# Performance work log

Hardware: AMD Instinct MI355X
Metric: run time of the kernel (lower is better)

The kernel has to match this reference:

```python
import jax, jax.numpy as jnp
import numpy as np

MAX_ITER = 3  # matches init kwarg max_iter


def setup_inputs() -> dict:
    key = jax.random.key(0)
    k1, k2, k3, k4 = jax.random.split(key, 4)
    B, S = 4, 160
    return {
        "s_edge": jax.random.normal(k1, (B, S, S), dtype=jnp.float32),
        "s_sib": jax.random.normal(k2, (B, S, S, S), dtype=jnp.float32),
        "s_cop": jax.random.normal(k3, (B, S, S, S), dtype=jnp.float32),
        "s_grd": jax.random.normal(k4, (B, S, S, S), dtype=jnp.float32),
        "mask": jnp.ones((B, S, S), dtype=bool),
    }


def reference(s_edge, s_sib, s_cop, s_grd, mask):
    B, S, _ = mask.shape
    idx = jnp.arange(S)
    # Permute to the [head, mod, (sib), batch] layout used by the torch code.
    mask_p = jnp.transpose(mask, (2, 1, 0))              # [h, m, B]
    # 2nd-order mask: both (h,m) and (h,t) arcs valid, and t != h, t != m
    pair_ok = mask_p[:, None, :, :] & mask_p[:, :, None, :]   # [h, m, t, B]
    t_ok = (idx[:, None, None] != idx[None, None, :]) & (
        idx[None, :, None] != idx[None, None, :])             # [h, m, t]
    mask2o = (pair_ok & t_ok[..., None]).astype(s_edge.dtype)  # [h, m, t, B]

    se = jnp.transpose(s_edge, (2, 1, 0))                 # [h, m, B]
    ss = jnp.transpose(s_sib, (2, 1, 3, 0)) * mask2o      # [h, m, t, B]
    sc = jnp.transpose(s_cop, (2, 1, 3, 0)) * mask2o
    sg = jnp.transpose(s_grd, (2, 1, 3, 0)) * mask2o

    q = jnp.zeros((2, S, S, B), dtype=se.dtype)
    for _ in range(MAX_ITER):
        q1 = jax.nn.softmax(q, axis=0)[1]                 # [h, m, B]
        # f[h,m,b] = sum_t q1[h,t,b]*ss + q1[t,m,b]*sc + q1[m,t,b]*sg
        f = (jnp.einsum('htb,hmtb->hmb', q1, ss)
             + jnp.einsum('tmb,hmtb->hmb', q1, sc)
             + jnp.einsum('mtb,hmtb->hmb', q1, sg))
        q = jnp.stack([jnp.zeros_like(f), se + f])        # [2, h, m, B]

    logQ = jax.nn.log_softmax(jnp.transpose(q, (3, 2, 1, 0)), axis=-1)  # [B, m, h... -> B,S,S,2]
    return jnp.exp(logQ)
```

## Files before the change

kernel.cpp:

```cpp
#include <hip/hip_runtime.h>
#include <cmath>

constexpr int S = 160;
constexpr int BATCH = 4;
constexpr int ZSPLIT = 2;
constexpr int ROWS = S / ZSPLIT;
constexpr int KC = S / 4;
constexpr int CHUNKS = ROWS * KC;
constexpr int TPB = 256;
constexpr int FULL_STEPS = CHUNKS / TPB;
constexpr int TAIL = CHUNKS - FULL_STEPS * TPB;

__device__ __forceinline__ float sigmoidf_(float x) {
  return 1.0f / (1.0f + expf(-x));
}

__global__ void prep_wf(const int* __restrict__ mask, unsigned char* __restrict__ wf) {
  int i = blockIdx.x * blockDim.x + threadIdx.x;
  if (i >= BATCH * S * S) return;
  int t = i % S;
  int bh = i / S;
  int h = bh % S;
  int b = bh / S;
  wf[i] = (mask[(b * S + t) * S + h] != 0 && t != h) ? 1 : 0;
}

template <bool FIRST, bool LAST>
__global__ __launch_bounds__(TPB, 5) void mfvi_iter(
    const float* __restrict__ s_edge,
    const float* __restrict__ s_sib,
    const float* __restrict__ s_cop,
    const float* __restrict__ s_grd,
    const int* __restrict__ mask,
    const unsigned char* __restrict__ wf,
    const float* __restrict__ q1_in,
    float* __restrict__ q1_out,
    float* __restrict__ outp) {
  const int m = blockIdx.x;
  const int b = blockIdx.y;
  const int z = blockIdx.z;
  const int tid = threadIdx.x;

  __shared__ __align__(16) float part[CHUNKS];
  __shared__ __align__(16) float colm[S];
  __shared__ __align__(16) float rowm[S];
  __shared__ float sef[ROWS];
  __shared__ float pmf[ROWS];

  const float* G = q1_in + (size_t)b * S * S;
  const size_t bm = (size_t)b * S + m;
  const int h0 = z * ROWS;

  if (tid < S) {
    if (!FIRST) {
      colm[tid] = G[tid * S + m];
      rowm[tid] = G[m * S + tid];
    }
    if (tid < ROWS) {
      sef[tid] = s_edge[bm * S + h0 + tid];
      pmf[tid] = (mask[bm * S + h0 + tid] != 0) ? 1.0f : 0.0f;
    }
  }
  __syncthreads();

  const size_t blk = (bm * S + h0) * (size_t)S;
  const float4* SS = (const float4*)(s_sib + blk);
  const float4* CC = (const float4*)(s_cop + blk);
  const float4* GG = (const float4*)(s_grd + blk);
  const float4* QQ = (const float4*)(G + h0 * S);
  const unsigned* WF = (const unsigned*)(wf + ((size_t)b * S + h0) * S);
  const int msel = m >> 2;
  const unsigned mclr = ~(255u << ((m & 3) * 8));

  auto body = [&](int c) {
    unsigned wu = WF[c];
    float4 s = SS[c];
    float4 cv = CC[c];
    float4 g = GG[c];
    int k = c % KC;
    if (k == msel) wu &= mclr;
    float w0 = (float)(wu & 255u);
    float w1 = (float)((wu >> 8) & 255u);
    float w2 = (float)((wu >> 16) & 255u);
    float w3 = (float)(wu >> 24);
    float p;
    if (FIRST) {
      float t0 = s.x + cv.x + g.x;
      float t1 = s.y + cv.y + g.y;
      float t2 = s.z + cv.z + g.z;
      float t3 = s.w + cv.w + g.w;
      p = fmaf(w0, t0, fmaf(w1, t1, fmaf(w2, t2, w3 * t3)));
    } else {
      float4 q = QQ[c];
      float4 cm = ((const float4*)colm)[k];
      float4 rm = ((const float4*)rowm)[k];
      float t0 = fmaf(q.x, s.x, fmaf(cm.x, cv.x, rm.x * g.x));
      float t1 = fmaf(q.y, s.y, fmaf(cm.y, cv.y, rm.y * g.y));
      float t2 = fmaf(q.z, s.z, fmaf(cm.z, cv.z, rm.z * g.z));
      float t3 = fmaf(q.w, s.w, fmaf(cm.w, cv.w, rm.w * g.w));
      p = fmaf(w0, t0, fmaf(w1, t1, fmaf(w2, t2, w3 * t3)));
    }
    part[c] = p;
  };

  for (int step = 0; step < FULL_STEPS; ++step) body(step * TPB + tid);
  if (tid < TAIL) body(FULL_STEPS * TPB + tid);
  __syncthreads();

  if (tid < ROWS) {
    const float4* pr = (const float4*)part + tid * (KC / 4);
    float4 a = pr[0];
#pragma unroll
    for (int i = 1; i < KC / 4; ++i) {
      float4 v = pr[i];
      a.x += v.x; a.y += v.y; a.z += v.z; a.w += v.w;
    }
    float acc = (a.x + a.y) + (a.z + a.w);
    const int h = h0 + tid;
    const float qv = fmaf(pmf[tid], FIRST ? 0.5f * acc : acc, sef[tid]);
    if (!LAST) {
      q1_out[((size_t)b * S + h) * S + m] = sigmoidf_(qv);
    } else {
      float2 o;
      o.x = sigmoidf_(-qv);
      o.y = sigmoidf_(qv);
      ((float2*)outp)[bm * S + h] = o;
    }
  }
}

extern "C" void kernel_launch(void* const* d_in, const int* in_sizes, int n_in,
                              void* d_out, int out_size, void* d_ws, size_t ws_size,
                              hipStream_t stream) {
  const float* s_edge = (const float*)d_in[0];
  const float* s_sib = (const float*)d_in[1];
  const float* s_cop = (const float*)d_in[2];
  const float* s_grd = (const float*)d_in[3];
  const int* mask = (const int*)d_in[4];
  float* outp = (float*)d_out;

  const int qn = BATCH * S * S;
  float* q1A = (float*)d_ws;
  float* q1B = q1A + qn;
  unsigned char* wf = (unsigned char*)(q1B + qn);

  prep_wf<<<(qn + 255) / 256, 256, 0, stream>>>(mask, wf);

  dim3 grid(S, BATCH, ZSPLIT);
  mfvi_iter<true, false><<<grid, TPB, 0, stream>>>(
      s_edge, s_sib, s_cop, s_grd, mask, wf, q1A, q1B, nullptr);
  mfvi_iter<false, false><<<grid, TPB, 0, stream>>>(
      s_edge, s_sib, s_cop, s_grd, mask, wf, q1B, q1A, nullptr);
  mfvi_iter<false, true><<<grid, TPB, 0, stream>>>(
      s_edge, s_sib, s_cop, s_grd, mask, wf, q1A, nullptr, outp);
}
```

Measured before the change: 261.2 us.

## Split rows four ways, pad reduction buffer, and batch paired streaming loads

Doubles the row split per (m, batch) so each block handles 40 rows, doubling the grid to 2560 blocks, and raises the launch-bounds occupancy hint from 5 to 8 blocks. Pads each row of the partial-sum shared buffer so the per-row float4 reduction reads hit fewer LDS bank conflicts. Unrolls the streaming loop so two chunks' loads are issued before either is computed, raising memory-level parallelism. In exchange, register pressure rises under the tighter occupancy bound, each block does less work, and the colm/rowm setup is repeated by twice as many blocks.

```diff
diff --git a/kernel.cpp b/kernel.cpp
--- a/kernel.cpp
+++ b/kernel.cpp
@@ -3,9 +3,10 @@
 
 constexpr int S = 160;
 constexpr int BATCH = 4;
-constexpr int ZSPLIT = 2;
+constexpr int ZSPLIT = 4;
 constexpr int ROWS = S / ZSPLIT;
 constexpr int KC = S / 4;
+constexpr int PSTR = KC + 4;
 constexpr int CHUNKS = ROWS * KC;
 constexpr int TPB = 256;
 constexpr int FULL_STEPS = CHUNKS / TPB;
@@ -26,7 +27,7 @@
 }
 
 template <bool FIRST, bool LAST>
-__global__ __launch_bounds__(TPB, 5) void mfvi_iter(
+__global__ __launch_bounds__(TPB, 8) void mfvi_iter(
     const float* __restrict__ s_edge,
     const float* __restrict__ s_sib,
     const float* __restrict__ s_cop,
@@ -41,7 +42,7 @@
   const int z = blockIdx.z;
   const int tid = threadIdx.x;
 
-  __shared__ __align__(16) float part[CHUNKS];
+  __shared__ __align__(16) float part[ROWS * PSTR];
   __shared__ __align__(16) float colm[S];
   __shared__ __align__(16) float rowm[S];
   __shared__ float sef[ROWS];
@@ -72,13 +73,12 @@
   const int msel = m >> 2;
   const unsigned mclr = ~(255u << ((m & 3) * 8));
 
-  auto body = [&](int c) {
-    unsigned wu = WF[c];
-    float4 s = SS[c];
-    float4 cv = CC[c];
-    float4 g = GG[c];
-    int k = c % KC;
-    if (k == msel) wu &= mclr;
+  auto compute = [&](int c, unsigned wu, const float4& s, const float4& cv,
+                     const float4& g) {
+    unsigned uc = (unsigned)c;
+    unsigned r = uc / (unsigned)KC;
+    unsigned k = uc - r * (unsigned)KC;
+    if ((int)k == msel) wu &= mclr;
     float w0 = (float)(wu & 255u);
     float w1 = (float)((wu >> 8) & 255u);
     float w2 = (float)((wu >> 16) & 255u);
@@ -100,15 +100,34 @@
       float t3 = fmaf(q.w, s.w, fmaf(cm.w, cv.w, rm.w * g.w));
       p = fmaf(w0, t0, fmaf(w1, t1, fmaf(w2, t2, w3 * t3)));
     }
-    part[c] = p;
+    part[r * PSTR + k] = p;
   };
 
-  for (int step = 0; step < FULL_STEPS; ++step) body(step * TPB + tid);
-  if (tid < TAIL) body(FULL_STEPS * TPB + tid);
+#pragma unroll
+  for (int sp = 0; sp < FULL_STEPS / 2; ++sp) {
+    const int c0 = (2 * sp) * TPB + tid;
+    const int c1 = c0 + TPB;
+    unsigned wu0 = WF[c0];
+    unsigned wu1 = WF[c1];
+    float4 s0 = SS[c0];
+    float4 s1 = SS[c1];
+    float4 cv0 = CC[c0];
+    float4 cv1 = CC[c1];
+    float4 g0 = GG[c0];
+    float4 g1 = GG[c1];
+    compute(c0, wu0, s0, cv0, g0);
+    compute(c1, wu1, s1, cv1, g1);
+  }
+  {
+    if (tid < TAIL) {
+      const int c = FULL_STEPS * TPB + tid;
+      compute(c, WF[c], SS[c], CC[c], GG[c]);
+    }
+  }
   __syncthreads();
 
   if (tid < ROWS) {
-    const float4* pr = (const float4*)part + tid * (KC / 4);
+    const float4* pr = (const float4*)(part + tid * PSTR);
     float4 a = pr[0];
 #pragma unroll
     for (int i = 1; i < KC / 4; ++i) {
```

After: 275.5 us. 5.4% more time.
